# Optimization experiments

Measured on AMD Instinct MI355X. Metric: run time of the kernel, lower is better.

The kernel has to match this reference:

```python
import jax, jax.numpy as jnp
import numpy as np
from jax import lax

B, C, H, W = 2, 256, 128, 128
NC, NP = 80, 9  # num_classes, num_points (3x3 dcn kernel)
PAD = 1


def conv2d(x, w, b=None, pad=1):
    out = lax.conv_general_dilated(x, w, (1, 1), [(pad, pad), (pad, pad)],
                                   dimension_numbers=('NCHW', 'OIHW', 'NCHW'))
    if b is not None:
        out = out + b[None, :, None, None]
    return out


def bilinear_sample(img_bhwc, py, px):
    # zero-padded bilinear sampling; py/px: [B,H,W] float coords
    Hi, Wi = img_bhwc.shape[1], img_bhwc.shape[2]
    y0 = jnp.floor(py)
    x0 = jnp.floor(px)
    wy1 = py - y0
    wx1 = px - x0

    def gather(yc, xc, w):
        valid = (yc >= 0) & (yc <= Hi - 1) & (xc >= 0) & (xc <= Wi - 1)
        yi = jnp.clip(yc, 0, Hi - 1).astype(jnp.int32)
        xi = jnp.clip(xc, 0, Wi - 1).astype(jnp.int32)
        v = jax.vmap(lambda im, yy, xx: im[yy, xx])(img_bhwc, yi, xi)  # [B,H,W,C]
        return v * (w * valid)[..., None]

    return (gather(y0, x0, (1 - wy1) * (1 - wx1)) + gather(y0, x0 + 1, (1 - wy1) * wx1)
            + gather(y0 + 1, x0, wy1 * (1 - wx1)) + gather(y0 + 1, x0 + 1, wy1 * wx1))


def deform_conv(x, offset, weight, mask=None, pad=1):
    # x: [B,C,H,W]; offset: [B,2K,H,W] interleaved (dy,dx) per kernel point;
    # mask: [B,K,H,W] or None (modulated DCN multiplies sampled value by mask as-is)
    kh, kw = weight.shape[2], weight.shape[3]
    xb = jnp.transpose(x, (0, 2, 3, 1))  # [B,H,W,C]
    gy, gx = jnp.meshgrid(jnp.arange(x.shape[2], dtype=x.dtype),
                          jnp.arange(x.shape[3], dtype=x.dtype), indexing='ij')
    acc = 0.
    for k in range(kh * kw):  # fixed structural loop over 9 kernel points
        ky, kx = k // kw, k % kw
        py = gy[None] + (ky - pad) + offset[:, 2 * k]
        px = gx[None] + (kx - pad) + offset[:, 2 * k + 1]
        val = bilinear_sample(xb, py, px)  # [B,H,W,C]
        if mask is not None:
            val = val * mask[:, k][..., None]
        acc = acc + jnp.einsum('bhwc,oc->bohw', val, weight[:, :, ky, kx])
    return acc


def setup_inputs() -> dict:
    key = jax.random.key(0)
    ks = jax.random.split(key, 16)
    d = {"x": jax.random.normal(ks[0], (B, C, H, W), jnp.float32)}

    def w(k, shape):
        return jax.random.normal(k, shape, jnp.float32) * 0.01

    i = 1
    for j in range(3):
        d[f"cls_w{j}"] = w(ks[i], (C, C, 3, 3)); i += 1
        d[f"cls_b{j}"] = jnp.zeros((C,), jnp.float32)
        d[f"reg_w{j}"] = w(ks[i], (C, C, 3, 3)); i += 1
        d[f"reg_b{j}"] = jnp.zeros((C,), jnp.float32)
    d["init_conv_w"] = w(ks[i], (C, C, 3, 3)); i += 1
    d["init_conv_b"] = jnp.zeros((C,), jnp.float32)
    d["init_out_w"] = w(ks[i], (3 * NP, C, 1, 1)); i += 1
    d["init_out_b"] = jnp.zeros((3 * NP,), jnp.float32)
    d["dcn_cls_w"] = w(ks[i], (C, C, 3, 3)); i += 1  # ModulatedDeformConv (bias=False)
    d["cls_out_w"] = w(ks[i], (NC, C, 1, 1)); i += 1
    d["cls_out_b"] = jnp.full((NC,), -4.59511985013459, jnp.float32)  # bias_init_with_prob(0.01)
    d["dcn_ref_w"] = w(ks[i], (C, C, 3, 3)); i += 1  # DeformConv (bias=False)
    d["ref_out_w"] = w(ks[i], (2 * NP, C, 1, 1)); i += 1
    d["ref_out_b"] = jnp.zeros((2 * NP,), jnp.float32)
    return d


def reference(x, cls_w0, cls_b0, reg_w0, reg_b0, cls_w1, cls_b1, reg_w1, reg_b1,
              cls_w2, cls_b2, reg_w2, reg_b2, init_conv_w, init_conv_b,
              init_out_w, init_out_b, dcn_cls_w, cls_out_w, cls_out_b,
              dcn_ref_w, ref_out_w, ref_out_b):
    relu = jax.nn.relu
    cls_feat = x
    for wgt, b in ((cls_w0, cls_b0), (cls_w1, cls_b1), (cls_w2, cls_b2)):
        cls_feat = relu(conv2d(cls_feat, wgt, b, 1))
    pts_feat = x
    for wgt, b in ((reg_w0, reg_b0), (reg_w1, reg_b1), (reg_w2, reg_b2)):
        pts_feat = relu(conv2d(pts_feat, wgt, b, 1))

    pts_out_init = conv2d(relu(conv2d(pts_feat, init_conv_w, init_conv_b, 1)),
                          init_out_w, init_out_b, 0)  # [B,27,H,W]
    o1, o2, mask = (pts_out_init[:, :NP], pts_out_init[:, NP:2 * NP],
                    pts_out_init[:, 2 * NP:])
    offset = jnp.concatenate([o1, o2], axis=1)  # dcn_offset (points_init = 0)

    cls_out = conv2d(relu(deform_conv(cls_feat, offset, dcn_cls_w, mask)),
                     cls_out_w, cls_out_b, 0)
    pts_out_refine = conv2d(relu(deform_conv(pts_feat, offset, dcn_ref_w)),
                            ref_out_w, ref_out_b, 0)
    pts_out_refine = pts_out_refine + lax.stop_gradient(offset)

    # pts2wh_offsets
    pts = pts_out_refine.reshape(B, NP, 2, H, W)
    pts_mean = pts.mean(axis=1, keepdims=True)          # [B,1,2,H,W]
    wh = jnp.abs(pts + pts_mean).max(axis=1)            # [B,2,H,W]
    reg = pts_mean[:, 0]                                # [B,2,H,W]
    return (cls_out, wh, reg)
```

## Files before the change

### kernel.cpp

```cpp
#include <hip/hip_runtime.h>

#define Bn 2
#define Cn 256
#define Hn 128
#define Wn 128
#define HWn 16384
#define NCn 80

typedef __attribute__((ext_vector_type(4))) float f32x4;
typedef __attribute__((ext_vector_type(8))) short bf16x8;

__device__ __forceinline__ float b2f(unsigned short h) {
    union { unsigned u; float f; } x; x.u = ((unsigned)h) << 16; return x.f;
}
__device__ __forceinline__ unsigned short f2bf(float f) {
    union { float f; unsigned u; } x; x.f = f;
    unsigned u = x.u + 0x7fffu + ((x.u >> 16) & 1u);
    return (unsigned short)(u >> 16);
}
__device__ __forceinline__ void unp8(int4 v, float* o) {
    const unsigned* u = (const unsigned*)&v;
#pragma unroll
    for (int i = 0; i < 4; ++i) {
        union { unsigned u; float f; } a, b;
        a.u = u[i] << 16;          o[2 * i]     = a.f;
        b.u = u[i] & 0xffff0000u;  o[2 * i + 1] = b.f;
    }
}

#define GLOAD16(gp, lp) __builtin_amdgcn_global_load_lds( \
    (__attribute__((address_space(1))) unsigned int*)(gp), \
    (__attribute__((address_space(3))) unsigned int*)(lp), 16, 0, 0)

__global__ void zeroK(unsigned short* z) { z[threadIdx.x] = 0; }

__global__ __launch_bounds__(256) void xinK(const float* __restrict__ x,
                                            unsigned short* __restrict__ o) {
    __shared__ float tb[32][33];
    const int b = blockIdx.z;
    const int hw0 = blockIdx.x * 32, c0 = blockIdx.y * 32;
    const int tx = threadIdx.x & 31, ty = threadIdx.x >> 5;
    const float* ip = x + ((size_t)(b * Cn + c0)) * HWn + hw0;
#pragma unroll
    for (int r = 0; r < 4; ++r) tb[ty + 8 * r][tx] = ip[(size_t)(ty + 8 * r) * HWn + tx];
    __syncthreads();
    unsigned short* op = o + ((size_t)(b * HWn + hw0)) * Cn + c0;
#pragma unroll
    for (int r = 0; r < 4; ++r) op[(size_t)(ty + 8 * r) * Cn + tx] = f2bf(tb[tx][ty + 8 * r]);
}

__global__ __launch_bounds__(256) void repack3(const float* __restrict__ w,
                                               unsigned short* __restrict__ o) {
    int t = blockIdx.x * 256 + threadIdx.x;
    int ic = t & 255, oc = (t >> 8) & 255, k = t >> 16;
    o[t] = f2bf(w[((size_t)(oc * Cn + ic)) * 9 + k]);
}

template <int OC, int PM>
__global__ __launch_bounds__(256) void repackHead(const float* __restrict__ w,
                                                  unsigned short* __restrict__ o) {
    int t = blockIdx.x * 256 + threadIdx.x;
    int ic = t & 255, oc = t >> 8;
    o[t] = (oc < OC) ? f2bf(w[(size_t)oc * Cn + ic]) : (unsigned short)0;
}

__global__ __launch_bounds__(256, 2) void convGemm(const unsigned short* __restrict__ feat,
                                                   const unsigned short* __restrict__ Wp,
                                                   const float* __restrict__ bias,
                                                   const unsigned short* __restrict__ zb,
                                                   unsigned short* __restrict__ out) {
    __shared__ __align__(16) unsigned short lA[128 * 64];
    __shared__ __align__(16) unsigned short lB[128 * 64];
    const int tid = threadIdx.x;
    const int l = tid & 63, w = tid >> 6;
    const int w_oc = w & 1, w_px = w >> 1;
    const int ry = blockIdx.x;
    const int b = ry >> 7, y = ry & 127;
    const int oc0 = blockIdx.y * 128;
    const int lr = l & 15, lg = l >> 4;

    int rI[4], cI[4], dI[4];
#pragma unroll
    for (int i = 0; i < 4; ++i) {
        int ps = (i * 4 + w) * 64 + l;
        rI[i] = ps >> 3;
        cI[i] = ((ps & 7) ^ (rI[i] & 7)) * 8;
        dI[i] = (i * 4 + w) * 512;
    }

    f32x4 acc[4][4];
#pragma unroll
    for (int i = 0; i < 4; ++i)
#pragma unroll
        for (int j = 0; j < 4; ++j) acc[i][j] = (f32x4){0.f, 0.f, 0.f, 0.f};

#pragma unroll 1
    for (int k = 0; k < 9; ++k) {
        const int dy = k / 3 - 1, dx = k % 3 - 1;
        const int yy = y + dy;
        const bool vy = (unsigned)yy < (unsigned)Hn;
        const size_t fbase = ((size_t)(b * Hn + yy)) * Wn;
#pragma unroll 1
        for (int cc = 0; cc < 4; ++cc) {
            const int c0 = cc * 64;
            const unsigned short* wk = Wp + (size_t)k * 65536 + (size_t)oc0 * Cn + c0;
#pragma unroll
            for (int i = 0; i < 4; ++i)
                GLOAD16(wk + rI[i] * Cn + cI[i], &lA[dI[i]]);
#pragma unroll
            for (int i = 0; i < 4; ++i) {
                const int pxs = rI[i] + dx;
                const unsigned short* g = (vy && (unsigned)pxs < (unsigned)Wn)
                    ? feat + ((fbase + pxs) * Cn + c0 + cI[i])
                    : zb;
                GLOAD16(g, &lB[dI[i]]);
            }
            __syncthreads();
#pragma unroll
            for (int h = 0; h < 2; ++h) {
                bf16x8 av[4], bv[4];
#pragma unroll
                for (int fm = 0; fm < 4; ++fm) {
                    const int row = w_oc * 64 + fm * 16 + lr;
                    const int ch = h * 4 + lg;
                    av[fm] = *(const bf16x8*)&lA[row * 64 + ((ch ^ (row & 7)) * 8)];
                }
#pragma unroll
                for (int fn = 0; fn < 4; ++fn) {
                    const int row = w_px * 64 + fn * 16 + lr;
                    const int ch = h * 4 + lg;
                    bv[fn] = *(const bf16x8*)&lB[row * 64 + ((ch ^ (row & 7)) * 8)];
                }
#pragma unroll
                for (int fm = 0; fm < 4; ++fm)
#pragma unroll
                    for (int fn = 0; fn < 4; ++fn)
                        acc[fm][fn] = __builtin_amdgcn_mfma_f32_16x16x32_bf16(
                            av[fm], bv[fn], acc[fm][fn], 0, 0, 0);
            }
            __syncthreads();
        }
    }

#pragma unroll
    for (int fm = 0; fm < 4; ++fm) {
        const int ocb = oc0 + w_oc * 64 + fm * 16 + lg * 4;
        const float b0 = bias[ocb], b1 = bias[ocb + 1], b2 = bias[ocb + 2], b3 = bias[ocb + 3];
#pragma unroll
        for (int fn = 0; fn < 4; ++fn) {
            const int px = w_px * 64 + fn * 16 + lr;
            f32x4 v = acc[fm][fn];
            unsigned u0 = (unsigned)f2bf(fmaxf(v[0] + b0, 0.f)) | ((unsigned)f2bf(fmaxf(v[1] + b1, 0.f)) << 16);
            unsigned u1 = (unsigned)f2bf(fmaxf(v[2] + b2, 0.f)) | ((unsigned)f2bf(fmaxf(v[3] + b3, 0.f)) << 16);
            uint2 st; st.x = u0; st.y = u1;
            *(uint2*)&out[((size_t)ry * Wn + px) * Cn + ocb] = st;
        }
    }
}

template <bool HASMASK>
__global__ __launch_bounds__(512, 2) void dcnGemm(const unsigned short* __restrict__ feat,
                                                  const float* __restrict__ o27,
                                                  const unsigned short* __restrict__ Wp,
                                                  unsigned short* __restrict__ out) {
    __shared__ __align__(16) unsigned short lA[256 * 64];
    __shared__ __align__(16) unsigned short lB[128 * 64];
    const int tid = threadIdx.x;
    const int l = tid & 63, w = tid >> 6;
    const int w_oc = w & 3, w_px = w >> 2;
    const int ry = blockIdx.x;
    const int b = ry >> 7, y = ry & 127;
    const int lr = l & 15, lg = l >> 4;

    int rI[4], cI[4], dI[4];
#pragma unroll
    for (int i = 0; i < 4; ++i) {
        int ps = (i * 8 + w) * 64 + l;
        rI[i] = ps >> 3;
        cI[i] = ((ps & 7) ^ (rI[i] & 7)) * 8;
        dI[i] = (i * 8 + w) * 512;
    }

    const int sp = tid >> 2;
    const int pc0 = (tid & 3) * 2;

    f32x4 acc[4][4];
#pragma unroll
    for (int i = 0; i < 4; ++i)
#pragma unroll
        for (int j = 0; j < 4; ++j) acc[i][j] = (f32x4){0.f, 0.f, 0.f, 0.f};

    const unsigned short* fb = feat + (size_t)b * HWn * Cn;
    const float* ob = o27 + (size_t)b * 27 * HWn + y * Wn + sp;

#pragma unroll 1
    for (int k = 0; k < 9; ++k) {
        const float offy = ob[(size_t)(2 * k) * HWn];
        const float offx = ob[(size_t)(2 * k + 1) * HWn];
        const float m = HASMASK ? ob[(size_t)(18 + k) * HWn] : 1.f;
        const float py = (float)(y + k / 3 - 1) + offy;
        const float px = (float)(sp + k % 3 - 1) + offx;
        const float y0f = floorf(py), x0f = floorf(px);
        const float wy1 = py - y0f, wx1 = px - x0f;
        const int iy0 = (int)y0f, ix0 = (int)x0f;
        const int iy1 = iy0 + 1, ix1 = ix0 + 1;
        const bool vy0 = (unsigned)iy0 < (unsigned)Hn, vy1 = (unsigned)iy1 < (unsigned)Hn;
        const bool vx0 = (unsigned)ix0 < (unsigned)Wn, vx1 = (unsigned)ix1 < (unsigned)Wn;
        const int yc0 = min(max(iy0, 0), Hn - 1), yc1 = min(max(iy1, 0), Hn - 1);
        const int xc0 = min(max(ix0, 0), Wn - 1), xc1 = min(max(ix1, 0), Wn - 1);
        const float cw0 = (vy0 && vx0) ? (1.f - wy1) * (1.f - wx1) * m : 0.f;
        const float cw1 = (vy0 && vx1) ? (1.f - wy1) * wx1 * m : 0.f;
        const float cw2 = (vy1 && vx0) ? wy1 * (1.f - wx1) * m : 0.f;
        const float cw3 = (vy1 && vx1) ? wy1 * wx1 * m : 0.f;
        const int ci0 = (yc0 * Wn + xc0) * Cn;
        const int ci1 = (yc0 * Wn + xc1) * Cn;
        const int ci2 = (yc1 * Wn + xc0) * Cn;
        const int ci3 = (yc1 * Wn + xc1) * Cn;

#pragma unroll 1
        for (int cc = 0; cc < 4; ++cc) {
            const int c0 = cc * 64;
            const unsigned short* wk = Wp + (size_t)k * 65536 + c0;
#pragma unroll
            for (int i = 0; i < 4; ++i)
                GLOAD16(wk + rI[i] * Cn + cI[i], &lA[dI[i]]);
#pragma unroll
            for (int s = 0; s < 2; ++s) {
                const int pcS = pc0 + s;
                const int cb = c0 + ((pcS ^ (sp & 7)) * 8);
                int4 q0 = *(const int4*)(fb + ci0 + cb);
                int4 q1 = *(const int4*)(fb + ci1 + cb);
                int4 q2 = *(const int4*)(fb + ci2 + cb);
                int4 q3 = *(const int4*)(fb + ci3 + cb);
                float f0[8], f1[8], f2[8], f3[8];
                unp8(q0, f0); unp8(q1, f1); unp8(q2, f2); unp8(q3, f3);
                unsigned u[4];
#pragma unroll
                for (int jj = 0; jj < 4; ++jj) {
                    float e0 = cw0 * f0[2 * jj] + cw1 * f1[2 * jj] + cw2 * f2[2 * jj] + cw3 * f3[2 * jj];
                    float e1 = cw0 * f0[2 * jj + 1] + cw1 * f1[2 * jj + 1] + cw2 * f2[2 * jj + 1] + cw3 * f3[2 * jj + 1];
                    u[jj] = (unsigned)f2bf(e0) | ((unsigned)f2bf(e1) << 16);
                }
                int4 pk; pk.x = u[0]; pk.y = u[1]; pk.z = u[2]; pk.w = u[3];
                *(int4*)&lB[sp * 64 + pcS * 8] = pk;
            }
            __syncthreads();
#pragma unroll
            for (int h = 0; h < 2; ++h) {
                bf16x8 av[4], bv[4];
#pragma unroll
                for (int fm = 0; fm < 4; ++fm) {
                    const int row = w_oc * 64 + fm * 16 + lr;
                    const int ch = h * 4 + lg;
                    av[fm] = *(const bf16x8*)&lA[row * 64 + ((ch ^ (row & 7)) * 8)];
                }
#pragma unroll
                for (int fn = 0; fn < 4; ++fn) {
                    const int row = w_px * 64 + fn * 16 + lr;
                    const int ch = h * 4 + lg;
                    bv[fn] = *(const bf16x8*)&lB[row * 64 + ((ch ^ (row & 7)) * 8)];
                }
#pragma unroll
                for (int fm = 0; fm < 4; ++fm)
#pragma unroll
                    for (int fn = 0; fn < 4; ++fn)
                        acc[fm][fn] = __builtin_amdgcn_mfma_f32_16x16x32_bf16(
                            av[fm], bv[fn], acc[fm][fn], 0, 0, 0);
            }
            __syncthreads();
        }
    }

#pragma unroll
    for (int fm = 0; fm < 4; ++fm) {
        const int ocb = w_oc * 64 + fm * 16 + lg * 4;
#pragma unroll
        for (int fn = 0; fn < 4; ++fn) {
            const int px = w_px * 64 + fn * 16 + lr;
            f32x4 v = acc[fm][fn];
            unsigned u0 = (unsigned)f2bf(fmaxf(v[0], 0.f)) | ((unsigned)f2bf(fmaxf(v[1], 0.f)) << 16);
            unsigned u1 = (unsigned)f2bf(fmaxf(v[2], 0.f)) | ((unsigned)f2bf(fmaxf(v[3], 0.f)) << 16);
            uint2 st; st.x = u0; st.y = u1;
            *(uint2*)&out[((size_t)ry * Wn + px) * Cn + ocb] = st;
        }
    }
}

template <int OC, int PM, bool ADD>
__global__ __launch_bounds__(256, 2) void headGemm(const unsigned short* __restrict__ feat,
                                                   const unsigned short* __restrict__ Wp,
                                                   const float* __restrict__ bias,
                                                   float* __restrict__ out,
                                                   const float* __restrict__ add,
                                                   int addC) {
    constexpr int MF = PM / 16;
    constexpr int NA = PM * 8 / 256;
    __shared__ __align__(16) unsigned short lA[PM * 64];
    __shared__ __align__(16) unsigned short lB[128 * 64];
    const int tid = threadIdx.x;
    const int l = tid & 63, w = tid >> 6;
    const int ry = blockIdx.x;
    const int b = ry >> 7, y = ry & 127;
    const int lr = l & 15, lg = l >> 4;

    int rIA[NA], cIA[NA], dIA[NA];
#pragma unroll
    for (int i = 0; i < NA; ++i) {
        int ps = (i * 4 + w) * 64 + l;
        rIA[i] = ps >> 3;
        cIA[i] = ((ps & 7) ^ (rIA[i] & 7)) * 8;
        dIA[i] = (i * 4 + w) * 512;
    }
    int rIB[4], cIB[4], dIB[4];
#pragma unroll
    for (int i = 0; i < 4; ++i) {
        int ps = (i * 4 + w) * 64 + l;
        rIB[i] = ps >> 3;
        cIB[i] = ((ps & 7) ^ (rIB[i] & 7)) * 8;
        dIB[i] = (i * 4 + w) * 512;
    }

    f32x4 acc[MF][2];
#pragma unroll
    for (int i = 0; i < MF; ++i)
#pragma unroll
        for (int j = 0; j < 2; ++j) acc[i][j] = (f32x4){0.f, 0.f, 0.f, 0.f};

    const unsigned short* frow = feat + ((size_t)ry * Wn) * Cn;

#pragma unroll 1
    for (int cc = 0; cc < 4; ++cc) {
        const int c0 = cc * 64;
#pragma unroll
        for (int i = 0; i < NA; ++i)
            GLOAD16(Wp + (size_t)rIA[i] * Cn + c0 + cIA[i], &lA[dIA[i]]);
#pragma unroll
        for (int i = 0; i < 4; ++i)
            GLOAD16(frow + (size_t)rIB[i] * Cn + c0 + cIB[i], &lB[dIB[i]]);
        __syncthreads();
#pragma unroll
        for (int h = 0; h < 2; ++h) {
            const int ch = h * 4 + lg;
            bf16x8 av[MF], bv[2];
#pragma unroll
            for (int fm = 0; fm < MF; ++fm) {
                const int row = fm * 16 + lr;
                av[fm] = *(const bf16x8*)&lA[row * 64 + ((ch ^ (row & 7)) * 8)];
            }
#pragma unroll
            for (int fn = 0; fn < 2; ++fn) {
                const int row = w * 32 + fn * 16 + lr;
                bv[fn] = *(const bf16x8*)&lB[row * 64 + ((ch ^ (row & 7)) * 8)];
            }
#pragma unroll
            for (int fm = 0; fm < MF; ++fm)
#pragma unroll
                for (int fn = 0; fn < 2; ++fn)
                    acc[fm][fn] = __builtin_amdgcn_mfma_f32_16x16x32_bf16(
                        av[fm], bv[fn], acc[fm][fn], 0, 0, 0);
        }
        __syncthreads();
    }

#pragma unroll
    for (int fm = 0; fm < MF; ++fm) {
        const int ocb = fm * 16 + lg * 4;
        if (ocb >= OC) break;
#pragma unroll
        for (int j = 0; j < 4; ++j) {
            const int oc = ocb + j;
            if (oc >= OC) break;
            const float bs = bias[oc];
#pragma unroll
            for (int fn = 0; fn < 2; ++fn) {
                const int px = w * 32 + fn * 16 + lr;
                float r = acc[fm][fn][j] + bs;
                const size_t oidx = ((size_t)(b * OC + oc)) * HWn + y * Wn + px;
                if (ADD) r += add[((size_t)(b * addC + oc)) * HWn + y * Wn + px];
                out[oidx] = r;
            }
        }
    }
}

__global__ __launch_bounds__(256) void postK(const float* __restrict__ r18,
                                             float* __restrict__ wh,
                                             float* __restrict__ reg) {
    const int hw = (blockIdx.x & 63) * 256 + threadIdx.x;
    const int b = blockIdx.x >> 6;
    const float* p = r18 + (size_t)(b * 18) * HWn + hw;
    float v[18];
#pragma unroll
    for (int c = 0; c < 18; ++c) v[c] = p[(size_t)c * HWn];
    float s0 = 0.f, s1 = 0.f;
#pragma unroll
    for (int q = 0; q < 9; ++q) { s0 += v[2 * q]; s1 += v[2 * q + 1]; }
    float m0 = s0 * (1.f / 9.f), m1 = s1 * (1.f / 9.f);
    float w0 = 0.f, w1 = 0.f;
#pragma unroll
    for (int q = 0; q < 9; ++q) {
        w0 = fmaxf(w0, fabsf(v[2 * q] + m0));
        w1 = fmaxf(w1, fabsf(v[2 * q + 1] + m1));
    }
    wh[(size_t)(b * 2 + 0) * HWn + hw] = w0;
    wh[(size_t)(b * 2 + 1) * HWn + hw] = w1;
    reg[(size_t)(b * 2 + 0) * HWn + hw] = m0;
    reg[(size_t)(b * 2 + 1) * HWn + hw] = m1;
}

extern "C" void kernel_launch(void* const* d_in, const int* in_sizes, int n_in,
                              void* d_out, int out_size, void* d_ws, size_t ws_size,
                              hipStream_t stream) {
    const float* x           = (const float*)d_in[0];
    const float* cls_w0      = (const float*)d_in[1];
    const float* cls_b0      = (const float*)d_in[2];
    const float* reg_w0      = (const float*)d_in[3];
    const float* reg_b0      = (const float*)d_in[4];
    const float* cls_w1      = (const float*)d_in[5];
    const float* cls_b1      = (const float*)d_in[6];
    const float* reg_w1      = (const float*)d_in[7];
    const float* reg_b1      = (const float*)d_in[8];
    const float* cls_w2      = (const float*)d_in[9];
    const float* cls_b2      = (const float*)d_in[10];
    const float* reg_w2      = (const float*)d_in[11];
    const float* reg_b2      = (const float*)d_in[12];
    const float* init_conv_w = (const float*)d_in[13];
    const float* init_conv_b = (const float*)d_in[14];
    const float* init_out_w  = (const float*)d_in[15];
    const float* init_out_b  = (const float*)d_in[16];
    const float* dcn_cls_w   = (const float*)d_in[17];
    const float* cls_out_w   = (const float*)d_in[18];
    const float* cls_out_b   = (const float*)d_in[19];
    const float* dcn_ref_w   = (const float*)d_in[20];
    const float* ref_out_w   = (const float*)d_in[21];
    const float* ref_out_b   = (const float*)d_in[22];

    float* out = (float*)d_out;

    char* ws = (char*)d_ws;
    const size_t IMG = (size_t)Bn * HWn * Cn * sizeof(unsigned short);
    unsigned short* Xb  = (unsigned short*)ws; ws += IMG;
    unsigned short* T1  = (unsigned short*)ws; ws += IMG;
    unsigned short* T2  = (unsigned short*)ws; ws += IMG;
    unsigned short* CLS = (unsigned short*)ws; ws += IMG;
    unsigned short* PTS = (unsigned short*)ws; ws += IMG;
    float* O27 = (float*)ws; ws += (size_t)Bn * 27 * HWn * sizeof(float);
    float* R18 = (float*)ws; ws += (size_t)Bn * 18 * HWn * sizeof(float);
    const size_t WSZ = (size_t)9 * Cn * Cn;
    unsigned short* Wpk = (unsigned short*)ws; ws += 9 * WSZ * sizeof(unsigned short);
    unsigned short* Wh27 = (unsigned short*)ws; ws += 32 * Cn * sizeof(unsigned short);
    unsigned short* Wh80 = (unsigned short*)ws; ws += 96 * Cn * sizeof(unsigned short);
    unsigned short* Wh18 = (unsigned short*)ws; ws += 32 * Cn * sizeof(unsigned short);
    unsigned short* ZB = (unsigned short*)ws;  ws += 512;

    unsigned short* W_cls0 = Wpk + 0 * WSZ;
    unsigned short* W_cls1 = Wpk + 1 * WSZ;
    unsigned short* W_cls2 = Wpk + 2 * WSZ;
    unsigned short* W_reg0 = Wpk + 3 * WSZ;
    unsigned short* W_reg1 = Wpk + 4 * WSZ;
    unsigned short* W_reg2 = Wpk + 5 * WSZ;
    unsigned short* W_init = Wpk + 6 * WSZ;
    unsigned short* W_dcls = Wpk + 7 * WSZ;
    unsigned short* W_dref = Wpk + 8 * WSZ;

    const dim3 blk(256);
    const dim3 cgrd(256, 2);
    const dim3 xgrd(512, 8, Bn);

    zeroK<<<1, 128, 0, stream>>>(ZB);
    repack3<<<2304, blk, 0, stream>>>(cls_w0, W_cls0);
    repack3<<<2304, blk, 0, stream>>>(cls_w1, W_cls1);
    repack3<<<2304, blk, 0, stream>>>(cls_w2, W_cls2);
    repack3<<<2304, blk, 0, stream>>>(reg_w0, W_reg0);
    repack3<<<2304, blk, 0, stream>>>(reg_w1, W_reg1);
    repack3<<<2304, blk, 0, stream>>>(reg_w2, W_reg2);
    repack3<<<2304, blk, 0, stream>>>(init_conv_w, W_init);
    repack3<<<2304, blk, 0, stream>>>(dcn_cls_w, W_dcls);
    repack3<<<2304, blk, 0, stream>>>(dcn_ref_w, W_dref);
    repackHead<27, 32><<<32, blk, 0, stream>>>(init_out_w, Wh27);
    repackHead<80, 96><<<96, blk, 0, stream>>>(cls_out_w, Wh80);
    repackHead<18, 32><<<32, blk, 0, stream>>>(ref_out_w, Wh18);
    xinK<<<xgrd, blk, 0, stream>>>(x, Xb);

    convGemm<<<cgrd, blk, 0, stream>>>(Xb, W_cls0, cls_b0, ZB, T1);
    convGemm<<<cgrd, blk, 0, stream>>>(T1, W_cls1, cls_b1, ZB, T2);
    convGemm<<<cgrd, blk, 0, stream>>>(T2, W_cls2, cls_b2, ZB, CLS);
    convGemm<<<cgrd, blk, 0, stream>>>(Xb, W_reg0, reg_b0, ZB, T1);
    convGemm<<<cgrd, blk, 0, stream>>>(T1, W_reg1, reg_b1, ZB, T2);
    convGemm<<<cgrd, blk, 0, stream>>>(T2, W_reg2, reg_b2, ZB, PTS);
    convGemm<<<cgrd, blk, 0, stream>>>(PTS, W_init, init_conv_b, ZB, T1);
    headGemm<27, 32, false><<<256, blk, 0, stream>>>(T1, Wh27, init_out_b, O27, nullptr, 0);
    dcnGemm<true><<<256, dim3(512), 0, stream>>>(CLS, O27, W_dcls, T2);
    headGemm<80, 96, false><<<256, blk, 0, stream>>>(T2, Wh80, cls_out_b, out, nullptr, 0);
    dcnGemm<false><<<256, dim3(512), 0, stream>>>(PTS, O27, W_dref, T1);
    headGemm<18, 32, true><<<256, blk, 0, stream>>>(T1, Wh18, ref_out_b, R18, O27, 27);

    postK<<<128, blk, 0, stream>>>(R18,
                                   out + (size_t)Bn * NCn * HWn,
                                   out + (size_t)Bn * NCn * HWn + (size_t)Bn * 2 * HWn);
}
```

Measured before the change: 658.1 us.

## Double-buffer conv and DCN GEMMs, split DCN tiles, batch weight repacks

Conv and deformable-conv GEMM main loops become a single 36-step pipeline with double-buffered LDS, so the next stage's global loads (and bilinear sampling for DCN) are issued before the current stage's MFMAs. The DCN kernel now handles half a row (64 pixels) per block, doubling the grid and raising the occupancy hint to 4. Block indices are remapped across rows, presumably to improve cache locality. The many repack launches are merged into two kernels. Double buffering doubles LDS use, which may limit occupancy, and smaller DCN tiles reload the weight tile more often.

```diff
diff --git a/kernel.cpp b/kernel.cpp
--- a/kernel.cpp
+++ b/kernel.cpp
@@ -13,19 +13,16 @@
 __device__ __forceinline__ float b2f(unsigned short h) {
     union { unsigned u; float f; } x; x.u = ((unsigned)h) << 16; return x.f;
 }
+__device__ __forceinline__ float blo(unsigned u) {
+    union { unsigned u; float f; } x; x.u = u << 16; return x.f;
+}
+__device__ __forceinline__ float bhi(unsigned u) {
+    union { unsigned u; float f; } x; x.u = u & 0xffff0000u; return x.f;
+}
 __device__ __forceinline__ unsigned short f2bf(float f) {
     union { float f; unsigned u; } x; x.f = f;
     unsigned u = x.u + 0x7fffu + ((x.u >> 16) & 1u);
     return (unsigned short)(u >> 16);
-}
-__device__ __forceinline__ void unp8(int4 v, float* o) {
-    const unsigned* u = (const unsigned*)&v;
-#pragma unroll
-    for (int i = 0; i < 4; ++i) {
-        union { unsigned u; float f; } a, b;
-        a.u = u[i] << 16;          o[2 * i]     = a.f;
-        b.u = u[i] & 0xffff0000u;  o[2 * i + 1] = b.f;
-    }
 }
 
 #define GLOAD16(gp, lp) __builtin_amdgcn_global_load_lds( \
@@ -49,19 +46,23 @@
     for (int r = 0; r < 4; ++r) op[(size_t)(ty + 8 * r) * Cn + tx] = f2bf(tb[tx][ty + 8 * r]);
 }
 
-__global__ __launch_bounds__(256) void repack3(const float* __restrict__ w,
-                                               unsigned short* __restrict__ o) {
-    int t = blockIdx.x * 256 + threadIdx.x;
-    int ic = t & 255, oc = (t >> 8) & 255, k = t >> 16;
-    o[t] = f2bf(w[((size_t)(oc * Cn + ic)) * 9 + k]);
-}
-
-template <int OC, int PM>
-__global__ __launch_bounds__(256) void repackHead(const float* __restrict__ w,
-                                                  unsigned short* __restrict__ o) {
-    int t = blockIdx.x * 256 + threadIdx.x;
-    int ic = t & 255, oc = t >> 8;
-    o[t] = (oc < OC) ? f2bf(w[(size_t)oc * Cn + ic]) : (unsigned short)0;
+struct WPtrs { const float* p[9]; };
+__global__ __launch_bounds__(256) void repackAll(WPtrs wsrc, unsigned short* __restrict__ dst) {
+    const int widx = blockIdx.y;
+    const int t = blockIdx.x * 256 + threadIdx.x;
+    const int ic = t & 255, oc = (t >> 8) & 255, k = t >> 16;
+    dst[(size_t)widx * 589824 + t] = f2bf(wsrc.p[widx][((size_t)(oc * Cn + ic)) * 9 + k]);
+}
+
+struct HPtrs { const float* w[3]; };
+__global__ __launch_bounds__(256) void repackHeads(HPtrs hs, unsigned short* __restrict__ dst) {
+    const int t = blockIdx.x * 256 + threadIdx.x;
+    const int ic = t & 255, row = t >> 8;
+    int which, oc, OC;
+    if (row < 32)       { which = 0; oc = row;       OC = 27; }
+    else if (row < 128) { which = 1; oc = row - 32;  OC = 80; }
+    else                { which = 2; oc = row - 128; OC = 18; }
+    dst[t] = (oc < OC) ? f2bf(hs.w[which][(size_t)oc * Cn + ic]) : (unsigned short)0;
 }
 
 __global__ __launch_bounds__(256, 2) void convGemm(const unsigned short* __restrict__ feat,
@@ -69,12 +70,12 @@
                                                    const float* __restrict__ bias,
                                                    const unsigned short* __restrict__ zb,
                                                    unsigned short* __restrict__ out) {
-    __shared__ __align__(16) unsigned short lA[128 * 64];
-    __shared__ __align__(16) unsigned short lB[128 * 64];
+    __shared__ __align__(16) unsigned short lA[2][8192];
+    __shared__ __align__(16) unsigned short lB[2][8192];
     const int tid = threadIdx.x;
     const int l = tid & 63, w = tid >> 6;
     const int w_oc = w & 1, w_px = w >> 1;
-    const int ry = blockIdx.x;
+    const int ry = (blockIdx.x & 7) * 32 + (blockIdx.x >> 3);
     const int b = ry >> 7, y = ry & 127;
     const int oc0 = blockIdx.y * 128;
     const int lr = l & 15, lg = l >> 4;
@@ -94,52 +95,59 @@
 #pragma unroll
         for (int j = 0; j < 4; ++j) acc[i][j] = (f32x4){0.f, 0.f, 0.f, 0.f};
 
-#pragma unroll 1
-    for (int k = 0; k < 9; ++k) {
+    auto stage = [&](int p, int bufIdx) {
+        const int k = p >> 2, c0 = (p & 3) * 64;
         const int dy = k / 3 - 1, dx = k % 3 - 1;
         const int yy = y + dy;
         const bool vy = (unsigned)yy < (unsigned)Hn;
         const size_t fbase = ((size_t)(b * Hn + yy)) * Wn;
+        const unsigned short* wk = Wp + (size_t)k * 65536 + (size_t)oc0 * Cn + c0;
+        unsigned short* la = lA[bufIdx];
+        unsigned short* lb = lB[bufIdx];
+#pragma unroll
+        for (int i = 0; i < 4; ++i)
+            GLOAD16(wk + rI[i] * Cn + cI[i], la + dI[i]);
+#pragma unroll
+        for (int i = 0; i < 4; ++i) {
+            const int pxs = rI[i] + dx;
+            const unsigned short* g = (vy && (unsigned)pxs < (unsigned)Wn)
+                ? feat + ((fbase + pxs) * Cn + c0 + cI[i])
+                : zb;
+            GLOAD16(g, lb + dI[i]);
+        }
+    };
+
+    stage(0, 0);
+    __syncthreads();
+
 #pragma unroll 1
-        for (int cc = 0; cc < 4; ++cc) {
-            const int c0 = cc * 64;
-            const unsigned short* wk = Wp + (size_t)k * 65536 + (size_t)oc0 * Cn + c0;
-#pragma unroll
-            for (int i = 0; i < 4; ++i)
-                GLOAD16(wk + rI[i] * Cn + cI[i], &lA[dI[i]]);
-#pragma unroll
-            for (int i = 0; i < 4; ++i) {
-                const int pxs = rI[i] + dx;
-                const unsigned short* g = (vy && (unsigned)pxs < (unsigned)Wn)
-                    ? feat + ((fbase + pxs) * Cn + c0 + cI[i])
-                    : zb;
-                GLOAD16(g, &lB[dI[i]]);
-            }
-            __syncthreads();
-#pragma unroll
-            for (int h = 0; h < 2; ++h) {
-                bf16x8 av[4], bv[4];
-#pragma unroll
-                for (int fm = 0; fm < 4; ++fm) {
-                    const int row = w_oc * 64 + fm * 16 + lr;
-                    const int ch = h * 4 + lg;
-                    av[fm] = *(const bf16x8*)&lA[row * 64 + ((ch ^ (row & 7)) * 8)];
-                }
-#pragma unroll
-                for (int fn = 0; fn < 4; ++fn) {
-                    const int row = w_px * 64 + fn * 16 + lr;
-                    const int ch = h * 4 + lg;
-                    bv[fn] = *(const bf16x8*)&lB[row * 64 + ((ch ^ (row & 7)) * 8)];
-                }
-#pragma unroll
-                for (int fm = 0; fm < 4; ++fm)
-#pragma unroll
-                    for (int fn = 0; fn < 4; ++fn)
-                        acc[fm][fn] = __builtin_amdgcn_mfma_f32_16x16x32_bf16(
-                            av[fm], bv[fn], acc[fm][fn], 0, 0, 0);
-            }
-            __syncthreads();
-        }
+    for (int p = 0; p < 36; ++p) {
+        const int cur = p & 1;
+        if (p < 35) stage(p + 1, cur ^ 1);
+        const unsigned short* la = lA[cur];
+        const unsigned short* lb = lB[cur];
+#pragma unroll
+        for (int h = 0; h < 2; ++h) {
+            const int ch = h * 4 + lg;
+            bf16x8 av[4], bv[4];
+#pragma unroll
+            for (int fm = 0; fm < 4; ++fm) {
+                const int row = w_oc * 64 + fm * 16 + lr;
+                av[fm] = *(const bf16x8*)&la[row * 64 + ((ch ^ (row & 7)) * 8)];
+            }
+#pragma unroll
+            for (int fn = 0; fn < 4; ++fn) {
+                const int row = w_px * 64 + fn * 16 + lr;
+                bv[fn] = *(const bf16x8*)&lb[row * 64 + ((ch ^ (row & 7)) * 8)];
+            }
+#pragma unroll
+            for (int fm = 0; fm < 4; ++fm)
+#pragma unroll
+                for (int fn = 0; fn < 4; ++fn)
+                    acc[fm][fn] = __builtin_amdgcn_mfma_f32_16x16x32_bf16(
+                        av[fm], bv[fn], acc[fm][fn], 0, 0, 0);
+        }
+        __syncthreads();
     }
 
 #pragma unroll
@@ -159,47 +167,52 @@
 }
 
 template <bool HASMASK>
-__global__ __launch_bounds__(512, 2) void dcnGemm(const unsigned short* __restrict__ feat,
+__global__ __launch_bounds__(512, 4) void dcnGemm(const unsigned short* __restrict__ feat,
                                                   const float* __restrict__ o27,
                                                   const unsigned short* __restrict__ Wp,
                                                   unsigned short* __restrict__ out) {
-    __shared__ __align__(16) unsigned short lA[256 * 64];
-    __shared__ __align__(16) unsigned short lB[128 * 64];
+    __shared__ __align__(16) unsigned short lA[2][16384];
+    __shared__ __align__(16) unsigned short lB[2][4096];
     const int tid = threadIdx.x;
     const int l = tid & 63, w = tid >> 6;
     const int w_oc = w & 3, w_px = w >> 2;
-    const int ry = blockIdx.x;
+    const int g = (blockIdx.x & 7) * 64 + (blockIdx.x >> 3);
+    const int ry = g >> 1, st = g & 1;
     const int b = ry >> 7, y = ry & 127;
+    const int x0 = st * 64;
     const int lr = l & 15, lg = l >> 4;
 
-    int rI[4], cI[4], dI[4];
+    int rIA[4], cIA[4], dIA[4];
 #pragma unroll
     for (int i = 0; i < 4; ++i) {
         int ps = (i * 8 + w) * 64 + l;
-        rI[i] = ps >> 3;
-        cI[i] = ((ps & 7) ^ (rI[i] & 7)) * 8;
-        dI[i] = (i * 8 + w) * 512;
-    }
-
-    const int sp = tid >> 2;
-    const int pc0 = (tid & 3) * 2;
-
-    f32x4 acc[4][4];
+        rIA[i] = ps >> 3;
+        cIA[i] = ((ps & 7) ^ (rIA[i] & 7)) * 8;
+        dIA[i] = (i * 8 + w) * 512;
+    }
+
+    const int sp = tid >> 3;
+    const int pc = tid & 7;
+    const int xg = x0 + sp;
+
+    const float* ob = o27 + (size_t)b * 27 * HWn + y * Wn + xg;
+    const unsigned short* fb = feat + (size_t)b * HWn * Cn;
+
+    f32x4 acc[4][2];
 #pragma unroll
     for (int i = 0; i < 4; ++i)
 #pragma unroll
-        for (int j = 0; j < 4; ++j) acc[i][j] = (f32x4){0.f, 0.f, 0.f, 0.f};
-
-    const unsigned short* fb = feat + (size_t)b * HWn * Cn;
-    const float* ob = o27 + (size_t)b * 27 * HWn + y * Wn + sp;
-
-#pragma unroll 1
-    for (int k = 0; k < 9; ++k) {
+        for (int j = 0; j < 2; ++j) acc[i][j] = (f32x4){0.f, 0.f, 0.f, 0.f};
+
+    int ci0, ci1, ci2, ci3;
+    float cw0, cw1, cw2, cw3;
+
+    auto sampParams = [&](int k) {
         const float offy = ob[(size_t)(2 * k) * HWn];
         const float offx = ob[(size_t)(2 * k + 1) * HWn];
         const float m = HASMASK ? ob[(size_t)(18 + k) * HWn] : 1.f;
         const float py = (float)(y + k / 3 - 1) + offy;
-        const float px = (float)(sp + k % 3 - 1) + offx;
+        const float px = (float)(xg + k % 3 - 1) + offx;
         const float y0f = floorf(py), x0f = floorf(px);
         const float wy1 = py - y0f, wx1 = px - x0f;
         const int iy0 = (int)y0f, ix0 = (int)x0f;
@@ -208,80 +221,88 @@
         const bool vx0 = (unsigned)ix0 < (unsigned)Wn, vx1 = (unsigned)ix1 < (unsigned)Wn;
         const int yc0 = min(max(iy0, 0), Hn - 1), yc1 = min(max(iy1, 0), Hn - 1);
         const int xc0 = min(max(ix0, 0), Wn - 1), xc1 = min(max(ix1, 0), Wn - 1);
-        const float cw0 = (vy0 && vx0) ? (1.f - wy1) * (1.f - wx1) * m : 0.f;
-        const float cw1 = (vy0 && vx1) ? (1.f - wy1) * wx1 * m : 0.f;
-        const float cw2 = (vy1 && vx0) ? wy1 * (1.f - wx1) * m : 0.f;
-        const float cw3 = (vy1 && vx1) ? wy1 * wx1 * m : 0.f;
-        const int ci0 = (yc0 * Wn + xc0) * Cn;
-        const int ci1 = (yc0 * Wn + xc1) * Cn;
-        const int ci2 = (yc1 * Wn + xc0) * Cn;
-        const int ci3 = (yc1 * Wn + xc1) * Cn;
+        cw0 = (vy0 && vx0) ? (1.f - wy1) * (1.f - wx1) * m : 0.f;
+        cw1 = (vy0 && vx1) ? (1.f - wy1) * wx1 * m : 0.f;
+        cw2 = (vy1 && vx0) ? wy1 * (1.f - wx1) * m : 0.f;
+        cw3 = (vy1 && vx1) ? wy1 * wx1 * m : 0.f;
+        ci0 = (yc0 * Wn + xc0) * Cn;
+        ci1 = (yc0 * Wn + xc1) * Cn;
+        ci2 = (yc1 * Wn + xc0) * Cn;
+        ci3 = (yc1 * Wn + xc1) * Cn;
+    };
+
+    auto stage = [&](int p, int bufIdx) {
+        const int k = p >> 2, c0 = (p & 3) * 64;
+        const unsigned short* wk = Wp + (size_t)k * 65536 + c0;
+        unsigned short* la = lA[bufIdx];
+#pragma unroll
+        for (int i = 0; i < 4; ++i)
+            GLOAD16(wk + rIA[i] * Cn + cIA[i], la + dIA[i]);
+        if ((p & 3) == 0) sampParams(k);
+        const int cb = c0 + pc * 8;
+        int4 q0 = *(const int4*)(fb + ci0 + cb);
+        int4 q1 = *(const int4*)(fb + ci1 + cb);
+        int4 q2 = *(const int4*)(fb + ci2 + cb);
+        int4 q3 = *(const int4*)(fb + ci3 + cb);
+        unsigned u[4];
+#pragma unroll
+        for (int jj = 0; jj < 4; ++jj) {
+            const unsigned a0 = ((const unsigned*)&q0)[jj];
+            const unsigned a1 = ((const unsigned*)&q1)[jj];
+            const unsigned a2 = ((const unsigned*)&q2)[jj];
+            const unsigned a3 = ((const unsigned*)&q3)[jj];
+            float e0 = cw0 * blo(a0) + cw1 * blo(a1) + cw2 * blo(a2) + cw3 * blo(a3);
+            float e1 = cw0 * bhi(a0) + cw1 * bhi(a1) + cw2 * bhi(a2) + cw3 * bhi(a3);
+            u[jj] = (unsigned)f2bf(e0) | ((unsigned)f2bf(e1) << 16);
+        }
+        int4 pk; pk.x = u[0]; pk.y = u[1]; pk.z = u[2]; pk.w = u[3];
+        *(int4*)&lB[bufIdx][sp * 64 + ((pc ^ (sp & 7)) * 8)] = pk;
+    };
+
+    stage(0, 0);
+    __syncthreads();
 
 #pragma unroll 1
-        for (int cc = 0; cc < 4; ++cc) {
-            const int c0 = cc * 64;
-            const unsigned short* wk = Wp + (size_t)k * 65536 + c0;
-#pragma unroll
-            for (int i = 0; i < 4; ++i)
-                GLOAD16(wk + rI[i] * Cn + cI[i], &lA[dI[i]]);
-#pragma unroll
-            for (int s = 0; s < 2; ++s) {
-                const int pcS = pc0 + s;
-                const int cb = c0 + ((pcS ^ (sp & 7)) * 8);
-                int4 q0 = *(const int4*)(fb + ci0 + cb);
-                int4 q1 = *(const int4*)(fb + ci1 + cb);
-                int4 q2 = *(const int4*)(fb + ci2 + cb);
-                int4 q3 = *(const int4*)(fb + ci3 + cb);
-                float f0[8], f1[8], f2[8], f3[8];
-                unp8(q0, f0); unp8(q1, f1); unp8(q2, f2); unp8(q3, f3);
-                unsigned u[4];
-#pragma unroll
-                for (int jj = 0; jj < 4; ++jj) {
-                    float e0 = cw0 * f0[2 * jj] + cw1 * f1[2 * jj] + cw2 * f2[2 * jj] + cw3 * f3[2 * jj];
-                    float e1 = cw0 * f0[2 * jj + 1] + cw1 * f1[2 * jj + 1] + cw2 * f2[2 * jj + 1] + cw3 * f3[2 * jj + 1];
-                    u[jj] = (unsigned)f2bf(e0) | ((unsigned)f2bf(e1) << 16);
-                }
-                int4 pk; pk.x = u[0]; pk.y = u[1]; pk.z = u[2]; pk.w = u[3];
-                *(int4*)&lB[sp * 64 + pcS * 8] = pk;
-            }
-            __syncthreads();
-#pragma unroll
-            for (int h = 0; h < 2; ++h) {
-                bf16x8 av[4], bv[4];
-#pragma unroll
-                for (int fm = 0; fm < 4; ++fm) {
-                    const int row = w_oc * 64 + fm * 16 + lr;
-                    const int ch = h * 4 + lg;
-                    av[fm] = *(const bf16x8*)&lA[row * 64 + ((ch ^ (row & 7)) * 8)];
-                }
-#pragma unroll
-                for (int fn = 0; fn < 4; ++fn) {
-                    const int row = w_px * 64 + fn * 16 + lr;
-                    const int ch = h * 4 + lg;
-                    bv[fn] = *(const bf16x8*)&lB[row * 64 + ((ch ^ (row & 7)) * 8)];
-                }
-#pragma unroll
-                for (int fm = 0; fm < 4; ++fm)
-#pragma unroll
-                    for (int fn = 0; fn < 4; ++fn)
-                        acc[fm][fn] = __builtin_amdgcn_mfma_f32_16x16x32_bf16(
-                            av[fm], bv[fn], acc[fm][fn], 0, 0, 0);
-            }
-            __syncthreads();
-        }
+    for (int p = 0; p < 36; ++p) {
+        const int cur = p & 1;
+        if (p < 35) stage(p + 1, cur ^ 1);
+        const unsigned short* la = lA[cur];
+        const unsigned short* lb = lB[cur];
+#pragma unroll
+        for (int h = 0; h < 2; ++h) {
+            const int ch = h * 4 + lg;
+            bf16x8 av[4], bv[2];
+#pragma unroll
+            for (int fm = 0; fm < 4; ++fm) {
+                const int row = w_oc * 64 + fm * 16 + lr;
+                av[fm] = *(const bf16x8*)&la[row * 64 + ((ch ^ (row & 7)) * 8)];
+            }
+#pragma unroll
+            for (int fn = 0; fn < 2; ++fn) {
+                const int row = w_px * 32 + fn * 16 + lr;
+                bv[fn] = *(const bf16x8*)&lb[row * 64 + ((ch ^ (row & 7)) * 8)];
+            }
+#pragma unroll
+            for (int fm = 0; fm < 4; ++fm)
+#pragma unroll
+                for (int fn = 0; fn < 2; ++fn)
+                    acc[fm][fn] = __builtin_amdgcn_mfma_f32_16x16x32_bf16(
+                        av[fm], bv[fn], acc[fm][fn], 0, 0, 0);
+        }
+        __syncthreads();
     }
 
 #pragma unroll
     for (int fm = 0; fm < 4; ++fm) {
         const int ocb = w_oc * 64 + fm * 16 + lg * 4;
 #pragma unroll
-        for (int fn = 0; fn < 4; ++fn) {
-            const int px = w_px * 64 + fn * 16 + lr;
+        for (int fn = 0; fn < 2; ++fn) {
+            const int px = x0 + w_px * 32 + fn * 16 + lr;
             f32x4 v = acc[fm][fn];
             unsigned u0 = (unsigned)f2bf(fmaxf(v[0], 0.f)) | ((unsigned)f2bf(fmaxf(v[1], 0.f)) << 16);
             unsigned u1 = (unsigned)f2bf(fmaxf(v[2], 0.f)) | ((unsigned)f2bf(fmaxf(v[3], 0.f)) << 16);
-            uint2 st; st.x = u0; st.y = u1;
-            *(uint2*)&out[((size_t)ry * Wn + px) * Cn + ocb] = st;
+            uint2 stv; stv.x = u0; stv.y = u1;
+            *(uint2*)&out[((size_t)ry * Wn + px) * Cn + ocb] = stv;
         }
     }
 }
@@ -299,7 +320,7 @@
     __shared__ __align__(16) unsigned short lB[128 * 64];
     const int tid = threadIdx.x;
     const int l = tid & 63, w = tid >> 6;
-    const int ry = blockIdx.x;
+    const int ry = (blockIdx.x & 7) * 32 + (blockIdx.x >> 3);
     const int b = ry >> 7, y = ry & 127;
     const int lr = l & 15, lg = l >> 4;
 
@@ -448,9 +469,7 @@
     float* R18 = (float*)ws; ws += (size_t)Bn * 18 * HWn * sizeof(float);
     const size_t WSZ = (size_t)9 * Cn * Cn;
     unsigned short* Wpk = (unsigned short*)ws; ws += 9 * WSZ * sizeof(unsigned short);
-    unsigned short* Wh27 = (unsigned short*)ws; ws += 32 * Cn * sizeof(unsigned short);
-    unsigned short* Wh80 = (unsigned short*)ws; ws += 96 * Cn * sizeof(unsigned short);
-    unsigned short* Wh18 = (unsigned short*)ws; ws += 32 * Cn * sizeof(unsigned short);
+    unsigned short* WhAll = (unsigned short*)ws; ws += 160 * Cn * sizeof(unsigned short);
     unsigned short* ZB = (unsigned short*)ws;  ws += 512;
 
     unsigned short* W_cls0 = Wpk + 0 * WSZ;
@@ -462,24 +481,22 @@
     unsigned short* W_init = Wpk + 6 * WSZ;
     unsigned short* W_dcls = Wpk + 7 * WSZ;
     unsigned short* W_dref = Wpk + 8 * WSZ;
+    unsigned short* Wh27 = WhAll;
+    unsigned short* Wh80 = WhAll + 32 * Cn;
+    unsigned short* Wh18 = WhAll + 128 * Cn;
 
     const dim3 blk(256);
     const dim3 cgrd(256, 2);
     const dim3 xgrd(512, 8, Bn);
 
     zeroK<<<1, 128, 0, stream>>>(ZB);
-    repack3<<<2304, blk, 0, stream>>>(cls_w0, W_cls0);
-    repack3<<<2304, blk, 0, stream>>>(cls_w1, W_cls1);
-    repack3<<<2304, blk, 0, stream>>>(cls_w2, W_cls2);
-    repack3<<<2304, blk, 0, stream>>>(reg_w0, W_reg0);
-    repack3<<<2304, blk, 0, stream>>>(reg_w1, W_reg1);
-    repack3<<<2304, blk, 0, stream>>>(reg_w2, W_reg2);
-    repack3<<<2304, blk, 0, stream>>>(init_conv_w, W_init);
-    repack3<<<2304, blk, 0, stream>>>(dcn_cls_w, W_dcls);
-    repack3<<<2304, blk, 0, stream>>>(dcn_ref_w, W_dref);
-    repackHead<27, 32><<<32, blk, 0, stream>>>(init_out_w, Wh27);
-    repackHead<80, 96><<<96, blk, 0, stream>>>(cls_out_w, Wh80);
-    repackHead<18, 32><<<32, blk, 0, stream>>>(ref_out_w, Wh18);
+    WPtrs wp;
+    wp.p[0] = cls_w0; wp.p[1] = cls_w1; wp.p[2] = cls_w2;
+    wp.p[3] = reg_w0; wp.p[4] = reg_w1; wp.p[5] = reg_w2;
+    wp.p[6] = init_conv_w; wp.p[7] = dcn_cls_w; wp.p[8] = dcn_ref_w;
+    repackAll<<<dim3(2304, 9), blk, 0, stream>>>(wp, Wpk);
+    HPtrs hp; hp.w[0] = init_out_w; hp.w[1] = cls_out_w; hp.w[2] = ref_out_w;
+    repackHeads<<<160, blk, 0, stream>>>(hp, WhAll);
     xinK<<<xgrd, blk, 0, stream>>>(x, Xb);
 
     convGemm<<<cgrd, blk, 0, stream>>>(Xb, W_cls0, cls_b0, ZB, T1);
@@ -490,9 +507,9 @@
     convGemm<<<cgrd, blk, 0, stream>>>(T2, W_reg2, reg_b2, ZB, PTS);
     convGemm<<<cgrd, blk, 0, stream>>>(PTS, W_init, init_conv_b, ZB, T1);
     headGemm<27, 32, false><<<256, blk, 0, stream>>>(T1, Wh27, init_out_b, O27, nullptr, 0);
-    dcnGemm<true><<<256, dim3(512), 0, stream>>>(CLS, O27, W_dcls, T2);
+    dcnGemm<true><<<512, dim3(512), 0, stream>>>(CLS, O27, W_dcls, T2);
     headGemm<80, 96, false><<<256, blk, 0, stream>>>(T2, Wh80, cls_out_b, out, nullptr, 0);
-    dcnGemm<false><<<256, dim3(512), 0, stream>>>(PTS, O27, W_dref, T1);
+    dcnGemm<false><<<512, dim3(512), 0, stream>>>(PTS, O27, W_dref, T1);
     headGemm<18, 32, true><<<256, blk, 0, stream>>>(T1, Wh18, ref_out_b, R18, O27, 27);
 
     postK<<<128, blk, 0, stream>>>(R18,
```

After: 611.4 us. -7.1%, faster.
